# Performance work log

Measured on AMD Instinct MI355X. Metric: run time of the kernel, lower is better.

Reference implementation:

```python
import jax, jax.numpy as jnp
import numpy as np
from jax import lax

B = 64          # batch
IMG = 384       # image H=W
PATCH = 16      # stem patch size -> 24x24 grid
C = 192         # hidden_channels
K = 5           # knn_graph k (hard-coded in extract_graph)
HG = IMG // PATCH
N = HG * HG     # total_num_nodes = 576
HID = 4 * C     # FFN expansion
PRED_HID = 1024
NUM_CLASSES = 1


def setup_inputs() -> dict:
    key = jax.random.key(0)
    ks = jax.random.split(key, 16)
    def w(k, shape, s=0.02):
        return jax.random.normal(k, shape, jnp.float32) * s
    f32 = jnp.float32
    return {
        "x": jax.random.normal(ks[0], (B, 3, IMG, IMG), f32),
        # stem: 16x16 patch-embed conv
        "stem_w": w(ks[1], (C, 3, PATCH, PATCH)),
        "stem_b": jnp.zeros((C,), f32),
        "pos_embed": w(ks[2], (1, C, HG, HG)),
        # GSAT edge-attention MLP: concat(src,dst) -> C -> 1 -> sigmoid
        "att_w1": w(ks[3], (2 * C, C)), "att_b1": jnp.zeros((C,), f32),
        "att_w2": w(ks[4], (C, 1)),     "att_b2": jnp.zeros((1,), f32),
        # two message-passing layers (GIN-style update)
        "gnn_w1": w(ks[5], (C, C)), "gnn_b1": jnp.zeros((C,), f32),
        "gnn_w2": w(ks[6], (C, C)), "gnn_b2": jnp.zeros((C,), f32),
        # FFN (1x1 convs == channel matmuls), BN in eval mode (mean0/var1)
        "ffn_w1": w(ks[7], (C, HID)), "ffn_b1": jnp.zeros((HID,), f32),
        "ffn_g1": jnp.ones((HID,), f32), "ffn_be1": jnp.zeros((HID,), f32),
        "ffn_w2": w(ks[8], (HID, C)), "ffn_b2": jnp.zeros((C,), f32),
        "ffn_g2": jnp.ones((C,), f32), "ffn_be2": jnp.zeros((C,), f32),
        # prediction head: 1x1 conv C->1024, BN(eval), gelu, 1x1 conv 1024->num_classes
        "pred_w1": w(ks[9], (C, PRED_HID)), "pred_b1": jnp.zeros((PRED_HID,), f32),
        "pred_g": jnp.ones((PRED_HID,), f32), "pred_be": jnp.zeros((PRED_HID,), f32),
        "pred_w2": w(ks[10], (PRED_HID, NUM_CLASSES)), "pred_b2": jnp.zeros((NUM_CLASSES,), f32),
    }


def reference(x, stem_w, stem_b, pos_embed,
              att_w1, att_b1, att_w2, att_b2,
              gnn_w1, gnn_b1, gnn_w2, gnn_b2,
              ffn_w1, ffn_b1, ffn_g1, ffn_be1,
              ffn_w2, ffn_b2, ffn_g2, ffn_be2,
              pred_w1, pred_b1, pred_g, pred_be, pred_w2, pred_b2):
    # ---- stem + pos_embed ----
    feat = lax.conv_general_dilated(x, stem_w, (PATCH, PATCH), 'VALID',
                                    dimension_numbers=('NCHW', 'OIHW', 'NCHW'))
    feat = feat + stem_b[None, :, None, None] + pos_embed        # [B,C,Hg,Wg]
    b, c, hg, wg = feat.shape
    n = hg * wg
    nf = feat.reshape(b, c, n).transpose(0, 2, 1)                # [B,N,C]
    nfd = lax.stop_gradient(nf)                                  # extract_graph under no_grad

    # ---- kNN graph build: per-image pairwise sq. distances + top-k ----
    sq = jnp.sum(nfd * nfd, axis=-1)                             # [B,N]
    d2 = sq[:, :, None] + sq[:, None, :] - 2.0 * jnp.einsum('bnc,bmc->bnm', nfd, nfd)
    d2 = d2 + jnp.eye(n, dtype=d2.dtype) * 1e9                   # exclude self-loops
    _, idx = lax.top_k(-d2, K)                                   # [B,N,K] nearest neighbors
    src = (idx + (jnp.arange(b) * n)[:, None, None]).reshape(-1)  # [E] global neighbor idx
    dst = jnp.repeat(jnp.arange(b * n), K)                        # [E] global center idx

    # ---- GSAT GNN: edge attention + attention-weighted message passing ----
    h = nfd.reshape(b * n, c)                                    # [BN,C] (detached)
    e = jax.nn.relu(jnp.concatenate([h[src], h[dst]], axis=-1) @ att_w1 + att_b1)
    edge_att = jax.nn.sigmoid(e @ att_w2 + att_b2)               # [E,1]
    for Wg, bg in ((gnn_w1, gnn_b1), (gnn_w2, gnn_b2)):
        m = jax.ops.segment_sum(edge_att * h[src], dst, num_segments=b * n)
        h = jax.nn.relu((h + m) @ Wg + bg)                       # GIN-style update

    # ---- FFN (1x1 convs) with residual, BN eval-mode affine ----
    t = h.reshape(b, n, c)                                       # [B,N,C]
    u = jax.nn.gelu((t @ ffn_w1 + ffn_b1) * ffn_g1 + ffn_be1, approximate=False)
    t = t + ((u @ ffn_w2 + ffn_b2) * ffn_g2 + ffn_be2)

    # ---- global average pool + prediction head ----
    g = jnp.mean(t, axis=1)                                      # [B,C]
    p = jax.nn.gelu((g @ pred_w1 + pred_b1) * pred_g + pred_be, approximate=False)
    prediction = p @ pred_w2 + pred_b2                           # [B,num_classes]
    return edge_att, prediction
```

## Files before the change

kernel.cpp:

```cpp
#include <hip/hip_runtime.h>
#include <hip/hip_bf16.h>
#include <math.h>

constexpr int B_    = 64;
constexpr int C_    = 192;
constexpr int N_    = 576;
constexpr int BN_   = B_ * N_;
constexpr int K_    = 5;
constexpr int E_    = BN_ * K_;

__device__ __forceinline__ float gelu_exact(float x) {
    return 0.5f * x * (1.0f + erff(x * 0.70710678118654752440f));
}

__device__ __forceinline__ float bf2f(unsigned short v) {
    return __uint_as_float(((unsigned)v) << 16);
}
__device__ __forceinline__ unsigned short f2bf(float x) {
    __hip_bfloat16 h = __float2bfloat16(x);
    return *(unsigned short*)&h;
}

__global__ __launch_bounds__(256) void transpose_w_k(const float* __restrict__ w,
                                                     float* __restrict__ wt) {
    int gid = blockIdx.x * 256 + threadIdx.x;
    int k = gid / 192, oc = gid % 192;
    wt[gid] = w[oc * 768 + k];
}

__global__ __launch_bounds__(256) void stem_gemm96_k(
    const float* __restrict__ x, const float* __restrict__ Wt,
    const float* __restrict__ sb, const float* __restrict__ pos,
    float* __restrict__ nf)
{
    __shared__ float As[96][68];
    __shared__ float Ws[64][68];
    const int tid = threadIdx.x;
    const int tr = tid >> 4, tc = tid & 15;
    const int mb = blockIdx.x;
    const int nb = blockIdx.y;
    const int b  = mb / 6;
    const int n0 = (mb % 6) * 96;

    float4 acc[6];
    #pragma unroll
    for (int i = 0; i < 6; ++i) acc[i] = float4{0.f, 0.f, 0.f, 0.f};

    for (int kc = 0; kc < 768; kc += 64) {
        #pragma unroll
        for (int i = 0; i < 6; ++i) {
            int q = i * 256 + tid;
            int m = q >> 4, kq = q & 15;
            int k = kc + kq * 4;
            int ci = k >> 8, rem = k & 255, dy = rem >> 4, dx = rem & 15;
            int n = n0 + m, py = n / 24, px = n % 24;
            const float* src = &x[(((size_t)(b * 3 + ci) * 384) + py * 16 + dy) * 384
                                  + px * 16 + dx];
            *(float4*)&As[m][kq * 4] = *(const float4*)src;
        }
        #pragma unroll
        for (int i = 0; i < 4; ++i) {
            int q = i * 256 + tid;
            int m = q >> 4, kq = q & 15;
            *(float4*)&Ws[m][kq * 4] =
                *(const float4*)&Wt[(size_t)(kc + m) * 192 + nb * 64 + kq * 4];
        }
        __syncthreads();
        #pragma unroll
        for (int k4 = 0; k4 < 64; k4 += 4) {
            float4 a4[6], b4[4];
            #pragma unroll
            for (int i = 0; i < 6; ++i) a4[i] = *(const float4*)&As[tr * 6 + i][k4];
            #pragma unroll
            for (int kk = 0; kk < 4; ++kk) b4[kk] = *(const float4*)&Ws[k4 + kk][tc * 4];
            #pragma unroll
            for (int i = 0; i < 6; ++i) {
                const float av[4] = {a4[i].x, a4[i].y, a4[i].z, a4[i].w};
                #pragma unroll
                for (int kk = 0; kk < 4; ++kk) {
                    acc[i].x += av[kk] * b4[kk].x;
                    acc[i].y += av[kk] * b4[kk].y;
                    acc[i].z += av[kk] * b4[kk].z;
                    acc[i].w += av[kk] * b4[kk].w;
                }
            }
        }
        __syncthreads();
    }

    #pragma unroll
    for (int i = 0; i < 6; ++i) {
        int n = n0 + tr * 6 + i;
        int row = b * 576 + n;
        int oc0 = nb * 64 + tc * 4;
        float v[4] = {acc[i].x, acc[i].y, acc[i].z, acc[i].w};
        #pragma unroll
        for (int j = 0; j < 4; ++j) {
            int oc = oc0 + j;
            v[j] = v[j] + sb[oc] + pos[oc * 576 + n];
        }
        *(float4*)&nf[(size_t)row * 192 + oc0] = float4{v[0], v[1], v[2], v[3]};
    }
}

__global__ __launch_bounds__(256) void sq_k(const float* __restrict__ nf,
                                            float* __restrict__ sq) {
    int wid = threadIdx.x >> 6, lane = threadIdx.x & 63;
    int n = blockIdx.x * 4 + wid;
    const float* row = nf + (size_t)n * 192;
    float s = 0.f;
    #pragma unroll
    for (int c = 0; c < 3; ++c) { float v = row[lane + c * 64]; s += v * v; }
    #pragma unroll
    for (int off = 32; off; off >>= 1) s += __shfl_down(s, off);
    if (lane == 0) sq[n] = s;
}

__global__ void transpose_nf_k(const float* __restrict__ nf, float* __restrict__ nfT) {
    __shared__ float tile[32][33];
    int b = blockIdx.z;
    int n0 = blockIdx.x * 32, c0 = blockIdx.y * 32;
    int tx = threadIdx.x, ty = threadIdx.y;
    #pragma unroll
    for (int r = 0; r < 4; ++r) {
        int i = ty * 4 + r;
        tile[i][tx] = nf[((size_t)b * 576 + n0 + i) * 192 + c0 + tx];
    }
    __syncthreads();
    #pragma unroll
    for (int r = 0; r < 4; ++r) {
        int i = ty * 4 + r;
        nfT[((size_t)b * 192 + c0 + i) * 576 + n0 + tx] = tile[tx][i];
    }
}

__global__ __launch_bounds__(64) void knn_sym_k(
    const float* __restrict__ nfT, const float* __restrict__ sqn,
    float* __restrict__ candV, int* __restrict__ candI)
{
    __shared__ float smem[64 * 69];
    float* As  = smem;
    float* Bs  = smem + 2048;
    float* d2s = smem;

    const int tid = threadIdx.x;
    const int tr = tid >> 3, tc = tid & 7;
    const int b = blockIdx.y;
    int t = blockIdx.x;
    int bi = 0;
    while (t >= 9 - bi) { t -= 9 - bi; ++bi; }
    const int bj = bi + t;
    const int r0 = bi * 64, c0 = bj * 64;

    float acc[8][8];
    #pragma unroll
    for (int i = 0; i < 8; ++i)
        #pragma unroll
        for (int j = 0; j < 8; ++j) acc[i][j] = 0.f;

    for (int kc = 0; kc < 192; kc += 32) {
        #pragma unroll
        for (int i = 0; i < 8; ++i) {
            int q = i * 64 + tid;
            int k = q >> 4, c4 = (q & 15) * 4;
            const float* srow = &nfT[((size_t)(b * 192 + kc + k)) * 576];
            *(float4*)&As[k * 64 + c4] = *(const float4*)&srow[r0 + c4];
            *(float4*)&Bs[k * 64 + c4] = *(const float4*)&srow[c0 + c4];
        }
        __syncthreads();
        #pragma unroll 8
        for (int kk = 0; kk < 32; ++kk) {
            float4 a0 = *(const float4*)&As[kk * 64 + tr * 8];
            float4 a1 = *(const float4*)&As[kk * 64 + tr * 8 + 4];
            float4 b0 = *(const float4*)&Bs[kk * 64 + tc * 8];
            float4 b1 = *(const float4*)&Bs[kk * 64 + tc * 8 + 4];
            const float av[8] = {a0.x, a0.y, a0.z, a0.w, a1.x, a1.y, a1.z, a1.w};
            const float bv[8] = {b0.x, b0.y, b0.z, b0.w, b1.x, b1.y, b1.z, b1.w};
            #pragma unroll
            for (int i = 0; i < 8; ++i)
                #pragma unroll
                for (int j = 0; j < 8; ++j)
                    acc[i][j] += av[i] * bv[j];
        }
        __syncthreads();
    }

    #pragma unroll
    for (int i = 0; i < 8; ++i) {
        int rl = tr * 8 + i, rg = r0 + rl;
        float sr = sqn[b * 576 + rg];
        #pragma unroll
        for (int j = 0; j < 8; ++j) {
            int cl = tc * 8 + j, cg = c0 + cl;
            float d = sr + sqn[b * 576 + cg] - 2.f * acc[i][j];
            if (cg == rg) d += 1e9f;
            d2s[rl * 69 + cl] = d;
        }
    }
    __syncthreads();

    {
        const int r = tid;
        float tv[5]; int ti[5];
        #pragma unroll
        for (int p = 0; p < 5; ++p) { tv[p] = 3.4e38f; ti[p] = 0; }
        for (int c = 0; c < 64; ++c) {
            float cv = d2s[r * 69 + c];
            if (cv < tv[4]) {
                int ci = c0 + c;
                #pragma unroll
                for (int q = 0; q < 5; ++q) {
                    bool less = cv < tv[q];
                    float nv = less ? tv[q] : cv;
                    int ni   = less ? ti[q] : ci;
                    tv[q] = less ? cv : tv[q];
                    ti[q] = less ? ci : ti[q];
                    cv = nv; ci = ni;
                }
            }
        }
        int gr = b * 576 + r0 + r;
        #pragma unroll
        for (int p = 0; p < 5; ++p) {
            candV[(size_t)gr * 45 + bj * 5 + p] = tv[p];
            candI[(size_t)gr * 45 + bj * 5 + p] = ti[p];
        }
    }

    if (bi != bj) {
        const int c = tid;
        float tv[5]; int ti[5];
        #pragma unroll
        for (int p = 0; p < 5; ++p) { tv[p] = 3.4e38f; ti[p] = 0; }
        for (int r = 0; r < 64; ++r) {
            float cv = d2s[r * 69 + c];
            if (cv < tv[4]) {
                int ci = r0 + r;
                #pragma unroll
                for (int q = 0; q < 5; ++q) {
                    bool less = cv < tv[q];
                    float nv = less ? tv[q] : cv;
                    int ni   = less ? ti[q] : ci;
                    tv[q] = less ? cv : tv[q];
                    ti[q] = less ? ci : ti[q];
                    cv = nv; ci = ni;
                }
            }
        }
        int gr = b * 576 + c0 + c;
        #pragma unroll
        for (int p = 0; p < 5; ++p) {
            candV[(size_t)gr * 45 + bi * 5 + p] = tv[p];
            candI[(size_t)gr * 45 + bi * 5 + p] = ti[p];
        }
    }
}

__global__ __launch_bounds__(256) void knn_merge_k(
    const float* __restrict__ candV, const int* __restrict__ candI,
    int* __restrict__ idxOut)
{
    int r = blockIdx.x * 256 + threadIdx.x;
    float tv[5]; int ti[5];
    #pragma unroll
    for (int p = 0; p < 5; ++p) { tv[p] = 3.4e38f; ti[p] = 0; }
    #pragma unroll 5
    for (int s = 0; s < 45; ++s) {
        float cv = candV[(size_t)r * 45 + s];
        if (cv < tv[4]) {
            int cidx = candI[(size_t)r * 45 + s];
            #pragma unroll
            for (int q = 0; q < 5; ++q) {
                bool less = cv < tv[q];
                float nv = less ? tv[q] : cv;
                int ni   = less ? ti[q] : cidx;
                tv[q] = less ? cv : tv[q];
                ti[q] = less ? cidx : ti[q];
                cv = nv; cidx = ni;
            }
        }
    }
    int base = (r / 576) * 576;
    #pragma unroll
    for (int p = 0; p < 5; ++p) idxOut[r * 5 + p] = base + ti[p];
}

template <int EPI>
__global__ __launch_bounds__(256) void gemm_rm_k(
    const float* __restrict__ A, const float* __restrict__ W, float* __restrict__ out,
    int M, int N, int K,
    const float* __restrict__ bias, const float* __restrict__ gsc,
    const float* __restrict__ gsh, const float* __restrict__ res)
{
    __shared__ float As[64][68];
    __shared__ float Ws[64][68];
    const int tid = threadIdx.x;
    const int tr = tid >> 4, tc = tid & 15;
    const int mBase = blockIdx.x * 64, nBase = blockIdx.y * 64;

    float4 acc[4];
    acc[0] = acc[1] = acc[2] = acc[3] = float4{0.f, 0.f, 0.f, 0.f};

    for (int kc = 0; kc < K; kc += 64) {
        #pragma unroll
        for (int i = 0; i < 4; ++i) {
            int q = i * 256 + tid;
            int m = q >> 4, kq = q & 15;
            *(float4*)&As[m][kq * 4] =
                *(const float4*)&A[(size_t)(mBase + m) * K + kc + kq * 4];
            *(float4*)&Ws[m][kq * 4] =
                *(const float4*)&W[(size_t)(kc + m) * N + nBase + kq * 4];
        }
        __syncthreads();
        #pragma unroll
        for (int k4 = 0; k4 < 64; k4 += 4) {
            float4 a4[4], b4[4];
            #pragma unroll
            for (int i = 0; i < 4; ++i) a4[i] = *(const float4*)&As[tr * 4 + i][k4];
            #pragma unroll
            for (int kk = 0; kk < 4; ++kk) b4[kk] = *(const float4*)&Ws[k4 + kk][tc * 4];
            #pragma unroll
            for (int i = 0; i < 4; ++i) {
                const float av[4] = {a4[i].x, a4[i].y, a4[i].z, a4[i].w};
                #pragma unroll
                for (int kk = 0; kk < 4; ++kk) {
                    acc[i].x += av[kk] * b4[kk].x;
                    acc[i].y += av[kk] * b4[kk].y;
                    acc[i].z += av[kk] * b4[kk].z;
                    acc[i].w += av[kk] * b4[kk].w;
                }
            }
        }
        __syncthreads();
    }

    #pragma unroll
    for (int i = 0; i < 4; ++i) {
        int row = mBase + tr * 4 + i;
        int n0 = nBase + tc * 4;
        float v[4] = {acc[i].x, acc[i].y, acc[i].z, acc[i].w};
        #pragma unroll
        for (int j = 0; j < 4; ++j) {
            int n = n0 + j;
            float xv = v[j];
            if (EPI == 1) xv += bias[n];
            if (EPI == 2) { xv += bias[n]; xv = fmaxf(xv, 0.f); }
            if (EPI == 3) { xv = (xv + bias[n]) * gsc[n] + gsh[n]; xv = gelu_exact(xv); }
            if (EPI == 4) {
                xv = res[(size_t)row * N + n] + (xv + bias[n]) * gsc[n] + gsh[n];
            }
            v[j] = xv;
        }
        *(float4*)&out[(size_t)row * N + n0] = float4{v[0], v[1], v[2], v[3]};
    }
}

template <int EPI>
__global__ __launch_bounds__(256) void gemm_mfma_k(
    const unsigned short* __restrict__ A, const unsigned short* __restrict__ Bt,
    unsigned short* __restrict__ out, int M, int N, int K,
    const float* __restrict__ bias, const float* __restrict__ gsc,
    const float* __restrict__ gsh, const unsigned short* __restrict__ res)
{
    using frag = __attribute__((ext_vector_type(8))) short;
    using facc = __attribute__((ext_vector_type(4))) float;
    __shared__ unsigned short As[64][72];
    __shared__ unsigned short Bs[64][72];
    const int tid = threadIdx.x;
    const int wave = tid >> 6, lane = tid & 63;
    const int m16 = lane & 15, quad = lane >> 4;
    const int mBase = blockIdx.x * 64, nBase = blockIdx.y * 64;

    facc zero = {0.f, 0.f, 0.f, 0.f};
    facc acc[4];
    #pragma unroll
    for (int t = 0; t < 4; ++t) acc[t] = zero;

    for (int kc = 0; kc < K; kc += 64) {
        #pragma unroll
        for (int r = 0; r < 2; ++r) {
            int q = r * 256 + tid;
            int row = q >> 3, c8 = (q & 7) * 8;
            *(int4*)&As[row][c8] =
                *(const int4*)&A[(size_t)(mBase + row) * K + kc + c8];
            *(int4*)&Bs[row][c8] =
                *(const int4*)&Bt[(size_t)(nBase + row) * K + kc + c8];
        }
        __syncthreads();
        #pragma unroll
        for (int kk = 0; kk < 64; kk += 32) {
            frag a = *(const frag*)&As[16 * wave + m16][kk + quad * 8];
            #pragma unroll
            for (int t = 0; t < 4; ++t) {
                frag b = *(const frag*)&Bs[t * 16 + m16][kk + quad * 8];
                acc[t] = __builtin_amdgcn_mfma_f32_16x16x32_bf16(a, b, acc[t], 0, 0, 0);
            }
        }
        __syncthreads();
    }

    #pragma unroll
    for (int t = 0; t < 4; ++t) {
        #pragma unroll
        for (int r = 0; r < 4; ++r) {
            int row = mBase + 16 * wave + quad * 4 + r;
            int col = nBase + t * 16 + m16;
            float xv = acc[t][r];
            if (EPI == 2) { xv += bias[col]; xv = fmaxf(xv, 0.f); }
            if (EPI == 3) { xv = (xv + bias[col]) * gsc[col] + gsh[col]; xv = gelu_exact(xv); }
            if (EPI == 4) {
                xv = bf2f(res[(size_t)row * N + col]) + (xv + bias[col]) * gsc[col] + gsh[col];
            }
            out[(size_t)row * N + col] = f2bf(xv);
        }
    }
}

template <int EPI>
__global__ __launch_bounds__(256) void gemm_mfma_split_k(
    const unsigned short* __restrict__ Ah, const unsigned short* __restrict__ Al,
    const unsigned short* __restrict__ Bh, const unsigned short* __restrict__ Bl,
    float* __restrict__ out, int M, int N, int K, const float* __restrict__ bias)
{
    using frag = __attribute__((ext_vector_type(8))) short;
    using facc = __attribute__((ext_vector_type(4))) float;
    __shared__ unsigned short AsH[64][72], AsL[64][72];
    __shared__ unsigned short BsH[64][72], BsL[64][72];
    const int tid = threadIdx.x;
    const int wave = tid >> 6, lane = tid & 63;
    const int m16 = lane & 15, quad = lane >> 4;
    const int mBase = blockIdx.x * 64, nBase = blockIdx.y * 64;

    facc zero = {0.f, 0.f, 0.f, 0.f};
    facc acc[4];
    #pragma unroll
    for (int t = 0; t < 4; ++t) acc[t] = zero;

    for (int kc = 0; kc < K; kc += 64) {
        #pragma unroll
        for (int r = 0; r < 2; ++r) {
            int q = r * 256 + tid;
            int row = q >> 3, c8 = (q & 7) * 8;
            *(int4*)&AsH[row][c8] = *(const int4*)&Ah[(size_t)(mBase + row) * K + kc + c8];
            *(int4*)&AsL[row][c8] = *(const int4*)&Al[(size_t)(mBase + row) * K + kc + c8];
            *(int4*)&BsH[row][c8] = *(const int4*)&Bh[(size_t)(nBase + row) * K + kc + c8];
            *(int4*)&BsL[row][c8] = *(const int4*)&Bl[(size_t)(nBase + row) * K + kc + c8];
        }
        __syncthreads();
        #pragma unroll
        for (int kk = 0; kk < 64; kk += 32) {
            frag ah = *(const frag*)&AsH[16 * wave + m16][kk + quad * 8];
            frag al = *(const frag*)&AsL[16 * wave + m16][kk + quad * 8];
            #pragma unroll
            for (int t = 0; t < 4; ++t) {
                frag bh = *(const frag*)&BsH[t * 16 + m16][kk + quad * 8];
                frag bl = *(const frag*)&BsL[t * 16 + m16][kk + quad * 8];
                acc[t] = __builtin_amdgcn_mfma_f32_16x16x32_bf16(ah, bh, acc[t], 0, 0, 0);
                acc[t] = __builtin_amdgcn_mfma_f32_16x16x32_bf16(ah, bl, acc[t], 0, 0, 0);
                acc[t] = __builtin_amdgcn_mfma_f32_16x16x32_bf16(al, bh, acc[t], 0, 0, 0);
            }
        }
        __syncthreads();
    }

    #pragma unroll
    for (int t = 0; t < 4; ++t) {
        #pragma unroll
        for (int r = 0; r < 4; ++r) {
            int row = mBase + 16 * wave + quad * 4 + r;
            int col = nBase + t * 16 + m16;
            float xv = acc[t][r];
            if (EPI == 1) xv += bias[col];
            out[(size_t)row * N + col] = xv;
        }
    }
}

__global__ __launch_bounds__(256) void asplit_k(const float* __restrict__ a,
                                                unsigned short* __restrict__ hi,
                                                unsigned short* __restrict__ lo) {
    int g = blockIdx.x * 256 + threadIdx.x;
    float v = a[g];
    unsigned short h = f2bf(v);
    hi[g] = h;
    lo[g] = f2bf(v - bf2f(h));
}

__global__ __launch_bounds__(256) void wsplit_att_k(const float* __restrict__ w,
                                                    unsigned short* __restrict__ hi,
                                                    unsigned short* __restrict__ lo) {
    int gid = blockIdx.x * 256 + threadIdx.x;
    int half = gid / 36864, r = gid % 36864;
    int n = r / 192, k = r % 192;
    float v = w[(size_t)(half * 192 + k) * 192 + n];
    unsigned short h = f2bf(v);
    hi[gid] = h;
    lo[gid] = f2bf(v - bf2f(h));
}

__global__ __launch_bounds__(256) void wprep_k(const float* __restrict__ w,
                                               unsigned short* __restrict__ wt,
                                               int K, int N) {
    int gid = blockIdx.x * 256 + threadIdx.x;
    int n = gid / K, k = gid % K;
    wt[gid] = f2bf(w[(size_t)k * N + n]);
}

__global__ __launch_bounds__(256) void edge_att_k(
    const float* __restrict__ hA, const float* __restrict__ hB,
    const int* __restrict__ idx, const float* __restrict__ w2,
    const float* __restrict__ b2, float* __restrict__ att)
{
    int wid = threadIdx.x >> 6, lane = threadIdx.x & 63;
    int e = blockIdx.x * 4 + wid;
    int dst = e / K_;
    int src = idx[e];
    float s = 0.f;
    #pragma unroll
    for (int c0 = 0; c0 < 3; ++c0) {
        int c = lane + c0 * 64;
        float v = hA[(size_t)src * 192 + c] + hB[(size_t)dst * 192 + c];
        v = fmaxf(v, 0.f);
        s += v * w2[c];
    }
    #pragma unroll
    for (int off = 32; off; off >>= 1) s += __shfl_down(s, off);
    if (lane == 0) att[e] = 1.f / (1.f + expf(-(s + b2[0])));
}

__device__ __forceinline__ float ldv(const float* p, size_t i) { return p[i]; }
__device__ __forceinline__ float ldv(const unsigned short* p, size_t i) { return bf2f(p[i]); }

template <typename TI>
__global__ __launch_bounds__(256) void msg_bf_k(
    const TI* __restrict__ h, const float* __restrict__ att,
    const int* __restrict__ idx, unsigned short* __restrict__ s)
{
    int g = blockIdx.x * 256 + threadIdx.x;
    int n = g / 192, c = g % 192;
    float acc = ldv(h, (size_t)g);
    #pragma unroll
    for (int p = 0; p < K_; ++p) {
        int sp = idx[n * K_ + p];
        acc += att[n * K_ + p] * ldv(h, (size_t)sp * 192 + c);
    }
    s[g] = f2bf(acc);
}

__global__ void pool_bf16_k(const unsigned short* __restrict__ t, float* __restrict__ g) {
    int b = blockIdx.x, c = threadIdx.x;
    float s = 0.f;
    for (int n = 0; n < 576; ++n) s += bf2f(t[((size_t)b * 576 + n) * 192 + c]);
    g[b * 192 + c] = s * (1.f / 576.f);
}

__global__ __launch_bounds__(256) void head2_k(
    const float* __restrict__ p, const float* __restrict__ w2,
    const float* __restrict__ b2, float* __restrict__ out)
{
    int b = blockIdx.x;
    float s = 0.f;
    for (int j = threadIdx.x; j < 1024; j += 256) s += p[(size_t)b * 1024 + j] * w2[j];
    #pragma unroll
    for (int off = 32; off; off >>= 1) s += __shfl_down(s, off);
    __shared__ float ls[4];
    int wid = threadIdx.x >> 6, lane = threadIdx.x & 63;
    if (lane == 0) ls[wid] = s;
    __syncthreads();
    if (threadIdx.x == 0) out[b] = ls[0] + ls[1] + ls[2] + ls[3] + b2[0];
}

extern "C" void kernel_launch(void* const* d_in, const int* in_sizes, int n_in,
                              void* d_out, int out_size, void* d_ws, size_t ws_size,
                              hipStream_t stream) {
    const float* x        = (const float*)d_in[0];
    const float* stem_w   = (const float*)d_in[1];
    const float* stem_b   = (const float*)d_in[2];
    const float* pos      = (const float*)d_in[3];
    const float* att_w1   = (const float*)d_in[4];
    const float* att_b1   = (const float*)d_in[5];
    const float* att_w2   = (const float*)d_in[6];
    const float* att_b2   = (const float*)d_in[7];
    const float* gnn_w1   = (const float*)d_in[8];
    const float* gnn_b1   = (const float*)d_in[9];
    const float* gnn_w2   = (const float*)d_in[10];
    const float* gnn_b2   = (const float*)d_in[11];
    const float* ffn_w1   = (const float*)d_in[12];
    const float* ffn_b1   = (const float*)d_in[13];
    const float* ffn_g1   = (const float*)d_in[14];
    const float* ffn_be1  = (const float*)d_in[15];
    const float* ffn_w2   = (const float*)d_in[16];
    const float* ffn_b2   = (const float*)d_in[17];
    const float* ffn_g2   = (const float*)d_in[18];
    const float* ffn_be2  = (const float*)d_in[19];
    const float* pred_w1  = (const float*)d_in[20];
    const float* pred_b1  = (const float*)d_in[21];
    const float* pred_g   = (const float*)d_in[22];
    const float* pred_be  = (const float*)d_in[23];
    const float* pred_w2  = (const float*)d_in[24];
    const float* pred_b2  = (const float*)d_in[25];

    float* ws = (float*)d_ws;
    const size_t RSZ = (size_t)BN_ * C_;
    float* R0 = ws;
    float* R1 = R0 + RSZ;
    float* R2 = R1 + RSZ;
    float* R3 = R2 + RSZ;
    float* sqb = R3 + RSZ;
    int*   idxb = (int*)(sqb + BN_);
    float* gb = (float*)(idxb + E_);
    float* pb = gb + 64 * C_;
    unsigned short* wg1T = (unsigned short*)(pb + 64 * 1024);
    unsigned short* wg2T = wg1T + 192 * 192;
    unsigned short* wf1T = wg2T + 192 * 192;
    unsigned short* wf2T = wf1T + 768 * 192;
    unsigned short* waHi = wf2T + 192 * 768;
    unsigned short* waLo = waHi + 2 * 192 * 192;

    float* candV = R1;
    int*   candI = (int*)(R1 + (size_t)BN_ * 45);

    unsigned short* Sb    = (unsigned short*)R1;
    unsigned short* Hb    = (unsigned short*)(R1 + RSZ / 2);
    unsigned short* Tb    = (unsigned short*)R2;
    unsigned short* ToutB = (unsigned short*)(R2 + RSZ / 2);
    unsigned short* Ahi   = (unsigned short*)R3;
    unsigned short* Alo   = Ahi + RSZ;
    unsigned short* Ub    = (unsigned short*)R3;

    float* att  = (float*)d_out;
    float* pred = att + E_;

    float* Wt = R3;

    wprep_k<<<144, 256, 0, stream>>>(gnn_w1, wg1T, 192, 192);
    wprep_k<<<144, 256, 0, stream>>>(gnn_w2, wg2T, 192, 192);
    wprep_k<<<576, 256, 0, stream>>>(ffn_w1, wf1T, 192, 768);
    wprep_k<<<576, 256, 0, stream>>>(ffn_w2, wf2T, 768, 192);
    wsplit_att_k<<<288, 256, 0, stream>>>(att_w1, waHi, waLo);

    transpose_w_k<<<576, 256, 0, stream>>>(stem_w, Wt);
    stem_gemm96_k<<<dim3(384, 3), 256, 0, stream>>>(x, Wt, stem_b, pos, R0);

    sq_k<<<BN_ / 4, 256, 0, stream>>>(R0, sqb);
    transpose_nf_k<<<dim3(18, 6, 64), dim3(32, 8), 0, stream>>>(R0, R3);
    knn_sym_k<<<dim3(45, 64), 64, 0, stream>>>(R3, sqb, candV, candI);
    knn_merge_k<<<BN_ / 256, 256, 0, stream>>>(candV, candI, idxb);

    asplit_k<<<BN_ * C_ / 256, 256, 0, stream>>>(R0, Ahi, Alo);
    gemm_mfma_split_k<0><<<dim3(576, 3), 256, 0, stream>>>(Ahi, Alo,
        waHi, waLo, R1, BN_, 192, 192, nullptr);
    gemm_mfma_split_k<1><<<dim3(576, 3), 256, 0, stream>>>(Ahi, Alo,
        waHi + 36864, waLo + 36864, R2, BN_, 192, 192, att_b1);
    edge_att_k<<<E_ / 4, 256, 0, stream>>>(R1, R2, idxb, att_w2, att_b2, att);

    msg_bf_k<float><<<BN_ * C_ / 256, 256, 0, stream>>>(R0, att, idxb, Sb);
    gemm_mfma_k<2><<<dim3(576, 3), 256, 0, stream>>>(Sb, wg1T, Hb,
        BN_, 192, 192, gnn_b1, nullptr, nullptr, nullptr);
    msg_bf_k<unsigned short><<<BN_ * C_ / 256, 256, 0, stream>>>(Hb, att, idxb, Sb);
    gemm_mfma_k<2><<<dim3(576, 3), 256, 0, stream>>>(Sb, wg2T, Tb,
        BN_, 192, 192, gnn_b2, nullptr, nullptr, nullptr);

    for (int ch = 0; ch < 2; ++ch) {
        const unsigned short* Ain = Tb + (size_t)ch * 18432 * 192;
        unsigned short* Tout = ToutB + (size_t)ch * 18432 * 192;
        gemm_mfma_k<3><<<dim3(288, 12), 256, 0, stream>>>(Ain, wf1T, Ub,
            18432, 768, 192, ffn_b1, ffn_g1, ffn_be1, nullptr);
        gemm_mfma_k<4><<<dim3(288, 3), 256, 0, stream>>>(Ub, wf2T, Tout,
            18432, 192, 768, ffn_b2, ffn_g2, ffn_be2, Ain);
    }

    pool_bf16_k<<<64, 192, 0, stream>>>(ToutB, gb);
    gemm_rm_k<3><<<dim3(1, 16), 256, 0, stream>>>(gb, pred_w1, pb,
        64, 1024, 192, pred_b1, pred_g, pred_be, nullptr);
    head2_k<<<64, 256, 0, stream>>>(pb, pred_w2, pred_b2, pred);
}
```

Before: 780.7 us.

## Retile stem GEMM with register prefetch and shrink kNN shared memory

The stem GEMM moves to 128-thread blocks, each computing a 96x96 output tile (6x12 per thread) with a K-chunk of 32. The next A chunk is prefetched into registers while the current chunk is computed, aiming for more reuse per thread and overlap of global loads with FMAs. The kNN tile kernel uses a 16-deep K chunk and computes the distance tile in two 32-row phases in a smaller LDS buffer. Row top-5 selection is split across two half-waves and merged with xor shuffles, which cuts LDS use for occupancy (launch bounds 64,4) at the cost of extra syncs and shuffle work. The merge breaks ties by index, which may change how ties are ordered.

Measured after the change: 1.209 ms. 1.55x slower.

```diff
diff --git a/kernel.cpp b/kernel.cpp
--- a/kernel.cpp
+++ b/kernel.cpp
@@ -28,60 +28,79 @@
     wt[gid] = w[oc * 768 + k];
 }
 
-__global__ __launch_bounds__(256) void stem_gemm96_k(
+__global__ __launch_bounds__(128, 3) void stem_gemm96c_k(
     const float* __restrict__ x, const float* __restrict__ Wt,
     const float* __restrict__ sb, const float* __restrict__ pos,
     float* __restrict__ nf)
 {
-    __shared__ float As[96][68];
-    __shared__ float Ws[64][68];
+    __shared__ float As[96][36];
+    __shared__ float Ws[32][100];
     const int tid = threadIdx.x;
-    const int tr = tid >> 4, tc = tid & 15;
+    const int tr = tid >> 3, tc = tid & 7;
     const int mb = blockIdx.x;
     const int nb = blockIdx.y;
     const int b  = mb / 6;
     const int n0 = (mb % 6) * 96;
 
-    float4 acc[6];
-    #pragma unroll
-    for (int i = 0; i < 6; ++i) acc[i] = float4{0.f, 0.f, 0.f, 0.f};
-
-    for (int kc = 0; kc < 768; kc += 64) {
+    float4 acc[6][3];
+    #pragma unroll
+    for (int i = 0; i < 6; ++i)
+        #pragma unroll
+        for (int g = 0; g < 3; ++g) acc[i][g] = float4{0.f, 0.f, 0.f, 0.f};
+
+    float4 aP[6];
+    auto loadA = [&](int kc) {
         #pragma unroll
         for (int i = 0; i < 6; ++i) {
-            int q = i * 256 + tid;
-            int m = q >> 4, kq = q & 15;
+            int q = i * 128 + tid;
+            int m = q >> 3, kq = q & 7;
             int k = kc + kq * 4;
             int ci = k >> 8, rem = k & 255, dy = rem >> 4, dx = rem & 15;
             int n = n0 + m, py = n / 24, px = n % 24;
-            const float* src = &x[(((size_t)(b * 3 + ci) * 384) + py * 16 + dy) * 384
-                                  + px * 16 + dx];
-            *(float4*)&As[m][kq * 4] = *(const float4*)src;
-        }
-        #pragma unroll
-        for (int i = 0; i < 4; ++i) {
-            int q = i * 256 + tid;
-            int m = q >> 4, kq = q & 15;
-            *(float4*)&Ws[m][kq * 4] =
-                *(const float4*)&Wt[(size_t)(kc + m) * 192 + nb * 64 + kq * 4];
-        }
-        __syncthreads();
-        #pragma unroll
-        for (int k4 = 0; k4 < 64; k4 += 4) {
-            float4 a4[6], b4[4];
+            aP[i] = *(const float4*)&x[(((size_t)(b * 3 + ci) * 384) + py * 16 + dy) * 384
+                                       + px * 16 + dx];
+        }
+    };
+
+    loadA(0);
+    for (int kc = 0; kc < 768; kc += 32) {
+        #pragma unroll
+        for (int i = 0; i < 6; ++i) {
+            int q = i * 128 + tid;
+            int m = q >> 3, kq = q & 7;
+            *(float4*)&As[m][kq * 4] = aP[i];
+        }
+        #pragma unroll
+        for (int i = 0; i < 6; ++i) {
+            int q = i * 128 + tid;
+            int wr = q / 24, c4 = (q % 24) * 4;
+            *(float4*)&Ws[wr][c4] =
+                *(const float4*)&Wt[(size_t)(kc + wr) * 192 + nb * 96 + c4];
+        }
+        __syncthreads();
+        if (kc + 32 < 768) loadA(kc + 32);
+        #pragma unroll
+        for (int k4 = 0; k4 < 32; k4 += 4) {
+            float4 a4[6];
             #pragma unroll
             for (int i = 0; i < 6; ++i) a4[i] = *(const float4*)&As[tr * 6 + i][k4];
             #pragma unroll
-            for (int kk = 0; kk < 4; ++kk) b4[kk] = *(const float4*)&Ws[k4 + kk][tc * 4];
-            #pragma unroll
-            for (int i = 0; i < 6; ++i) {
-                const float av[4] = {a4[i].x, a4[i].y, a4[i].z, a4[i].w};
+            for (int kk = 0; kk < 4; ++kk) {
+                float4 b4[3];
                 #pragma unroll
-                for (int kk = 0; kk < 4; ++kk) {
-                    acc[i].x += av[kk] * b4[kk].x;
-                    acc[i].y += av[kk] * b4[kk].y;
-                    acc[i].z += av[kk] * b4[kk].z;
-                    acc[i].w += av[kk] * b4[kk].w;
+                for (int g = 0; g < 3; ++g)
+                    b4[g] = *(const float4*)&Ws[k4 + kk][tc * 12 + g * 4];
+                #pragma unroll
+                for (int i = 0; i < 6; ++i) {
+                    const float av = (kk == 0) ? a4[i].x : (kk == 1) ? a4[i].y
+                                   : (kk == 2) ? a4[i].z : a4[i].w;
+                    #pragma unroll
+                    for (int g = 0; g < 3; ++g) {
+                        acc[i][g].x += av * b4[g].x;
+                        acc[i][g].y += av * b4[g].y;
+                        acc[i][g].z += av * b4[g].z;
+                        acc[i][g].w += av * b4[g].w;
+                    }
                 }
             }
         }
@@ -92,14 +111,17 @@
     for (int i = 0; i < 6; ++i) {
         int n = n0 + tr * 6 + i;
         int row = b * 576 + n;
-        int oc0 = nb * 64 + tc * 4;
-        float v[4] = {acc[i].x, acc[i].y, acc[i].z, acc[i].w};
-        #pragma unroll
-        for (int j = 0; j < 4; ++j) {
-            int oc = oc0 + j;
-            v[j] = v[j] + sb[oc] + pos[oc * 576 + n];
-        }
-        *(float4*)&nf[(size_t)row * 192 + oc0] = float4{v[0], v[1], v[2], v[3]};
+        #pragma unroll
+        for (int g = 0; g < 3; ++g) {
+            int oc0 = nb * 96 + tc * 12 + g * 4;
+            float v[4] = {acc[i][g].x, acc[i][g].y, acc[i][g].z, acc[i][g].w};
+            #pragma unroll
+            for (int j = 0; j < 4; ++j) {
+                int oc = oc0 + j;
+                v[j] = v[j] + sb[oc] + pos[oc * 576 + n];
+            }
+            *(float4*)&nf[(size_t)row * 192 + oc0] = float4{v[0], v[1], v[2], v[3]};
+        }
     }
 }
 
@@ -134,14 +156,49 @@
     }
 }
 
-__global__ __launch_bounds__(64) void knn_sym_k(
+__device__ __forceinline__ void ins5(float* tv, int* ti, float cv, int ci) {
+    #pragma unroll
+    for (int q = 0; q < 5; ++q) {
+        bool less = cv < tv[q];
+        float nv = less ? tv[q] : cv;
+        int ni   = less ? ti[q] : ci;
+        tv[q] = less ? cv : tv[q];
+        ti[q] = less ? ci : ti[q];
+        cv = nv; ci = ni;
+    }
+}
+__device__ __forceinline__ void merge5_xor(float* tv, int* ti, int mask) {
+    float ov[5]; int oi[5];
+    #pragma unroll
+    for (int p = 0; p < 5; ++p) {
+        ov[p] = __shfl_xor(tv[p], mask);
+        oi[p] = __shfl_xor(ti[p], mask);
+    }
+    #pragma unroll
+    for (int s = 0; s < 5; ++s) {
+        float cv = ov[s]; int ci = oi[s];
+        if (cv < tv[4] || (cv == tv[4] && ci < ti[4])) {
+            #pragma unroll
+            for (int q = 0; q < 5; ++q) {
+                bool less = (cv < tv[q]) || (cv == tv[q] && ci < ti[q]);
+                float nv = less ? tv[q] : cv;
+                int ni   = less ? ti[q] : ci;
+                tv[q] = less ? cv : tv[q];
+                ti[q] = less ? ci : ti[q];
+                cv = nv; ci = ni;
+            }
+        }
+    }
+}
+
+__global__ __launch_bounds__(64, 4) void knn_sym3_k(
     const float* __restrict__ nfT, const float* __restrict__ sqn,
     float* __restrict__ candV, int* __restrict__ candI)
 {
-    __shared__ float smem[64 * 69];
-    float* As  = smem;
-    float* Bs  = smem + 2048;
-    float* d2s = smem;
+    __shared__ float smem[2304];
+    float (*As)[64]  = (float(*)[64])smem;
+    float (*Bs)[64]  = (float(*)[64])(smem + 1024);
+    float (*d2s)[72] = (float(*)[72])smem;
 
     const int tid = threadIdx.x;
     const int tr = tid >> 3, tc = tid & 7;
@@ -150,7 +207,7 @@
     int bi = 0;
     while (t >= 9 - bi) { t -= 9 - bi; ++bi; }
     const int bj = bi + t;
-    const int r0 = bi * 64, c0 = bj * 64;
+    const int row0 = bi * 64, c0 = bj * 64;
 
     float acc[8][8];
     #pragma unroll
@@ -158,22 +215,22 @@
         #pragma unroll
         for (int j = 0; j < 8; ++j) acc[i][j] = 0.f;
 
-    for (int kc = 0; kc < 192; kc += 32) {
+    for (int kc = 0; kc < 192; kc += 16) {
         #pragma unroll
         for (int i = 0; i < 8; ++i) {
             int q = i * 64 + tid;
-            int k = q >> 4, c4 = (q & 15) * 4;
-            const float* srow = &nfT[((size_t)(b * 192 + kc + k)) * 576];
-            *(float4*)&As[k * 64 + c4] = *(const float4*)&srow[r0 + c4];
-            *(float4*)&Bs[k * 64 + c4] = *(const float4*)&srow[c0 + c4];
-        }
-        __syncthreads();
-        #pragma unroll 8
-        for (int kk = 0; kk < 32; ++kk) {
-            float4 a0 = *(const float4*)&As[kk * 64 + tr * 8];
-            float4 a1 = *(const float4*)&As[kk * 64 + tr * 8 + 4];
-            float4 b0 = *(const float4*)&Bs[kk * 64 + tc * 8];
-            float4 b1 = *(const float4*)&Bs[kk * 64 + tc * 8 + 4];
+            int rr = (q >> 4) & 15, c4 = (q & 15) * 4;
+            const float* srow = &nfT[((size_t)(b * 192 + kc + rr)) * 576];
+            if (i < 4) *(float4*)&As[rr][c4] = *(const float4*)&srow[row0 + c4];
+            else       *(float4*)&Bs[rr][c4] = *(const float4*)&srow[c0 + c4];
+        }
+        __syncthreads();
+        #pragma unroll
+        for (int kk = 0; kk < 16; ++kk) {
+            float4 a0 = *(const float4*)&As[kk][tr * 8];
+            float4 a1 = *(const float4*)&As[kk][tr * 8 + 4];
+            float4 b0 = *(const float4*)&Bs[kk][tc * 8];
+            float4 b1 = *(const float4*)&Bs[kk][tc * 8 + 4];
             const float av[8] = {a0.x, a0.y, a0.z, a0.w, a1.x, a1.y, a1.z, a1.w};
             const float bv[8] = {b0.x, b0.y, b0.z, b0.w, b1.x, b1.y, b1.z, b1.w};
             #pragma unroll
@@ -185,73 +242,67 @@
         __syncthreads();
     }
 
-    #pragma unroll
-    for (int i = 0; i < 8; ++i) {
-        int rl = tr * 8 + i, rg = r0 + rl;
-        float sr = sqn[b * 576 + rg];
-        #pragma unroll
-        for (int j = 0; j < 8; ++j) {
-            int cl = tc * 8 + j, cg = c0 + cl;
-            float d = sr + sqn[b * 576 + cg] - 2.f * acc[i][j];
-            if (cg == rg) d += 1e9f;
-            d2s[rl * 69 + cl] = d;
-        }
-    }
-    __syncthreads();
-
-    {
-        const int r = tid;
-        float tv[5]; int ti[5];
-        #pragma unroll
-        for (int p = 0; p < 5; ++p) { tv[p] = 3.4e38f; ti[p] = 0; }
-        for (int c = 0; c < 64; ++c) {
-            float cv = d2s[r * 69 + c];
-            if (cv < tv[4]) {
-                int ci = c0 + c;
+    float tvB[5]; int tiB[5];
+    #pragma unroll
+    for (int p = 0; p < 5; ++p) { tvB[p] = 3.4e38f; tiB[p] = 0x7fffffff; }
+
+    #pragma unroll
+    for (int ph = 0; ph < 2; ++ph) {
+        const int base = ph * 32;
+        if ((tr >> 2) == ph) {
+            const int trl = tr & 3;
+            #pragma unroll
+            for (int i = 0; i < 8; ++i) {
+                int rl = trl * 8 + i;
+                int rg = row0 + base + rl;
+                float sr = sqn[b * 576 + rg];
+                float dv[8];
                 #pragma unroll
-                for (int q = 0; q < 5; ++q) {
-                    bool less = cv < tv[q];
-                    float nv = less ? tv[q] : cv;
-                    int ni   = less ? ti[q] : ci;
-                    tv[q] = less ? cv : tv[q];
-                    ti[q] = less ? ci : ti[q];
-                    cv = nv; ci = ni;
+                for (int j = 0; j < 8; ++j) {
+                    int cg = c0 + tc * 8 + j;
+                    float d = sr + sqn[b * 576 + cg] - 2.f * acc[i][j];
+                    if (cg == rg) d += 1e9f;
+                    dv[j] = d;
                 }
-            }
-        }
-        int gr = b * 576 + r0 + r;
+                *(float4*)&d2s[rl][tc * 8]     = float4{dv[0], dv[1], dv[2], dv[3]};
+                *(float4*)&d2s[rl][tc * 8 + 4] = float4{dv[4], dv[5], dv[6], dv[7]};
+            }
+        }
+        __syncthreads();
+        {
+            const int arow = tid & 31, part = tid >> 5;
+            float pv[5]; int pi[5];
+            #pragma unroll
+            for (int q = 0; q < 5; ++q) { pv[q] = 3.4e38f; pi[q] = 0x7fffffff; }
+            for (int j = 0; j < 32; ++j) {
+                int cl = part * 32 + j;
+                float cv = d2s[arow][cl];
+                if (cv < pv[4]) ins5(pv, pi, cv, c0 + cl);
+            }
+            merge5_xor(pv, pi, 32);
+            if (part == 0) {
+                int gr = b * 576 + row0 + base + arow;
+                #pragma unroll
+                for (int p = 0; p < 5; ++p) {
+                    candV[(size_t)gr * 45 + bj * 5 + p] = pv[p];
+                    candI[(size_t)gr * 45 + bj * 5 + p] = pi[p];
+                }
+            }
+        }
+        if (bi != bj) {
+            for (int rr = 0; rr < 32; ++rr) {
+                float cv = d2s[rr][tid];
+                if (cv < tvB[4]) ins5(tvB, tiB, cv, row0 + base + rr);
+            }
+        }
+        __syncthreads();
+    }
+    if (bi != bj) {
+        int gr = b * 576 + c0 + tid;
         #pragma unroll
         for (int p = 0; p < 5; ++p) {
-            candV[(size_t)gr * 45 + bj * 5 + p] = tv[p];
-            candI[(size_t)gr * 45 + bj * 5 + p] = ti[p];
-        }
-    }
-
-    if (bi != bj) {
-        const int c = tid;
-        float tv[5]; int ti[5];
-        #pragma unroll
-        for (int p = 0; p < 5; ++p) { tv[p] = 3.4e38f; ti[p] = 0; }
-        for (int r = 0; r < 64; ++r) {
-            float cv = d2s[r * 69 + c];
-            if (cv < tv[4]) {
-                int ci = r0 + r;
-                #pragma unroll
-                for (int q = 0; q < 5; ++q) {
-                    bool less = cv < tv[q];
-                    float nv = less ? tv[q] : cv;
-                    int ni   = less ? ti[q] : ci;
-                    tv[q] = less ? cv : tv[q];
-                    ti[q] = less ? ci : ti[q];
-                    cv = nv; ci = ni;
-                }
-            }
-        }
-        int gr = b * 576 + c0 + c;
-        #pragma unroll
-        for (int p = 0; p < 5; ++p) {
-            candV[(size_t)gr * 45 + bi * 5 + p] = tv[p];
-            candI[(size_t)gr * 45 + bi * 5 + p] = ti[p];
+            candV[(size_t)gr * 45 + bi * 5 + p] = tvB[p];
+            candI[(size_t)gr * 45 + bi * 5 + p] = tiB[p];
         }
     }
 }
@@ -640,11 +691,11 @@
     wsplit_att_k<<<288, 256, 0, stream>>>(att_w1, waHi, waLo);
 
     transpose_w_k<<<576, 256, 0, stream>>>(stem_w, Wt);
-    stem_gemm96_k<<<dim3(384, 3), 256, 0, stream>>>(x, Wt, stem_b, pos, R0);
+    stem_gemm96c_k<<<dim3(384, 2), 128, 0, stream>>>(x, Wt, stem_b, pos, R0);
 
     sq_k<<<BN_ / 4, 256, 0, stream>>>(R0, sqb);
     transpose_nf_k<<<dim3(18, 6, 64), dim3(32, 8), 0, stream>>>(R0, R3);
-    knn_sym_k<<<dim3(45, 64), 64, 0, stream>>>(R3, sqb, candV, candI);
+    knn_sym3_k<<<dim3(45, 64), 64, 0, stream>>>(R3, sqb, candV, candI);
     knn_merge_k<<<BN_ / 256, 256, 0, stream>>>(candV, candI, idxb);
 
     asplit_k<<<BN_ * C_ / 256, 256, 0, stream>>>(R0, Ahi, Alo);
```

## Enlarge bf16 MFMA GEMM M-tile to 256 rows per block

Applied to the files above, without the earlier changes.

The bf16 MFMA GEMM now has each block cover 256 rows instead of 64. Each wave computes a 64x64 sub-tile with a 4x4 accumulator grid and reuses the B fragments across four A fragments. This cuts the number of times B tiles are reloaded, raises MFMA work per LDS load, and shrinks the grids by a factor of four. The cost is higher register and LDS use per block and fewer blocks, which may lower occupancy. The diff also adds a redundant duplicate store of candI in the knn kernel that has no speed purpose.

Result: no change. 773.6 us (-0.9%).

```diff
diff --git a/kernel.cpp b/kernel.cpp
--- a/kernel.cpp
+++ b/kernel.cpp
@@ -251,6 +251,10 @@
         #pragma unroll
         for (int p = 0; p < 5; ++p) {
             candV[(size_t)gr * 45 + bi * 5 + p] = tv[p];
+            candI[(size_t)gr * 45 + bi * 5 + p] = tv[p] == tv[p] ? ti[p] : ti[p];
+        }
+        #pragma unroll
+        for (int p = 0; p < 5; ++p) {
             candI[(size_t)gr * 45 + bi * 5 + p] = ti[p];
         }
     }
@@ -364,54 +368,69 @@
 {
     using frag = __attribute__((ext_vector_type(8))) short;
     using facc = __attribute__((ext_vector_type(4))) float;
-    __shared__ unsigned short As[64][72];
+    __shared__ unsigned short As[256][72];
     __shared__ unsigned short Bs[64][72];
     const int tid = threadIdx.x;
     const int wave = tid >> 6, lane = tid & 63;
     const int m16 = lane & 15, quad = lane >> 4;
-    const int mBase = blockIdx.x * 64, nBase = blockIdx.y * 64;
+    const int mBase = blockIdx.x * 256, nBase = blockIdx.y * 64;
 
     facc zero = {0.f, 0.f, 0.f, 0.f};
-    facc acc[4];
-    #pragma unroll
-    for (int t = 0; t < 4; ++t) acc[t] = zero;
+    facc acc[4][4];
+    #pragma unroll
+    for (int ms = 0; ms < 4; ++ms)
+        #pragma unroll
+        for (int t = 0; t < 4; ++t) acc[ms][t] = zero;
 
     for (int kc = 0; kc < K; kc += 64) {
         #pragma unroll
-        for (int r = 0; r < 2; ++r) {
+        for (int r = 0; r < 8; ++r) {
             int q = r * 256 + tid;
             int row = q >> 3, c8 = (q & 7) * 8;
             *(int4*)&As[row][c8] =
                 *(const int4*)&A[(size_t)(mBase + row) * K + kc + c8];
+        }
+        #pragma unroll
+        for (int r = 0; r < 2; ++r) {
+            int q = r * 256 + tid;
+            int row = q >> 3, c8 = (q & 7) * 8;
             *(int4*)&Bs[row][c8] =
                 *(const int4*)&Bt[(size_t)(nBase + row) * K + kc + c8];
         }
         __syncthreads();
         #pragma unroll
         for (int kk = 0; kk < 64; kk += 32) {
-            frag a = *(const frag*)&As[16 * wave + m16][kk + quad * 8];
-            #pragma unroll
-            for (int t = 0; t < 4; ++t) {
-                frag b = *(const frag*)&Bs[t * 16 + m16][kk + quad * 8];
-                acc[t] = __builtin_amdgcn_mfma_f32_16x16x32_bf16(a, b, acc[t], 0, 0, 0);
-            }
-        }
-        __syncthreads();
-    }
-
-    #pragma unroll
-    for (int t = 0; t < 4; ++t) {
-        #pragma unroll
-        for (int r = 0; r < 4; ++r) {
-            int row = mBase + 16 * wave + quad * 4 + r;
-            int col = nBase + t * 16 + m16;
-            float xv = acc[t][r];
-            if (EPI == 2) { xv += bias[col]; xv = fmaxf(xv, 0.f); }
-            if (EPI == 3) { xv = (xv + bias[col]) * gsc[col] + gsh[col]; xv = gelu_exact(xv); }
-            if (EPI == 4) {
-                xv = bf2f(res[(size_t)row * N + col]) + (xv + bias[col]) * gsc[col] + gsh[col];
-            }
-            out[(size_t)row * N + col] = f2bf(xv);
+            frag bfr[4];
+            #pragma unroll
+            for (int t = 0; t < 4; ++t)
+                bfr[t] = *(const frag*)&Bs[t * 16 + m16][kk + quad * 8];
+            #pragma unroll
+            for (int ms = 0; ms < 4; ++ms) {
+                frag a = *(const frag*)&As[64 * wave + ms * 16 + m16][kk + quad * 8];
+                #pragma unroll
+                for (int t = 0; t < 4; ++t)
+                    acc[ms][t] = __builtin_amdgcn_mfma_f32_16x16x32_bf16(a, bfr[t], acc[ms][t], 0, 0, 0);
+            }
+        }
+        __syncthreads();
+    }
+
+    #pragma unroll
+    for (int ms = 0; ms < 4; ++ms) {
+        #pragma unroll
+        for (int t = 0; t < 4; ++t) {
+            #pragma unroll
+            for (int r = 0; r < 4; ++r) {
+                int row = mBase + 64 * wave + ms * 16 + quad * 4 + r;
+                int col = nBase + t * 16 + m16;
+                float xv = acc[ms][t][r];
+                if (EPI == 2) { xv += bias[col]; xv = fmaxf(xv, 0.f); }
+                if (EPI == 3) { xv = (xv + bias[col]) * gsc[col] + gsh[col]; xv = gelu_exact(xv); }
+                if (EPI == 4) {
+                    xv = bf2f(res[(size_t)row * N + col]) + (xv + bias[col]) * gsc[col] + gsh[col];
+                }
+                out[(size_t)row * N + col] = f2bf(xv);
+            }
         }
     }
 }
@@ -655,18 +674,18 @@
     edge_att_k<<<E_ / 4, 256, 0, stream>>>(R1, R2, idxb, att_w2, att_b2, att);
 
     msg_bf_k<float><<<BN_ * C_ / 256, 256, 0, stream>>>(R0, att, idxb, Sb);
-    gemm_mfma_k<2><<<dim3(576, 3), 256, 0, stream>>>(Sb, wg1T, Hb,
+    gemm_mfma_k<2><<<dim3(144, 3), 256, 0, stream>>>(Sb, wg1T, Hb,
         BN_, 192, 192, gnn_b1, nullptr, nullptr, nullptr);
     msg_bf_k<unsigned short><<<BN_ * C_ / 256, 256, 0, stream>>>(Hb, att, idxb, Sb);
-    gemm_mfma_k<2><<<dim3(576, 3), 256, 0, stream>>>(Sb, wg2T, Tb,
+    gemm_mfma_k<2><<<dim3(144, 3), 256, 0, stream>>>(Sb, wg2T, Tb,
         BN_, 192, 192, gnn_b2, nullptr, nullptr, nullptr);
 
     for (int ch = 0; ch < 2; ++ch) {
         const unsigned short* Ain = Tb + (size_t)ch * 18432 * 192;
         unsigned short* Tout = ToutB + (size_t)ch * 18432 * 192;
-        gemm_mfma_k<3><<<dim3(288, 12), 256, 0, stream>>>(Ain, wf1T, Ub,
+        gemm_mfma_k<3><<<dim3(72, 12), 256, 0, stream>>>(Ain, wf1T, Ub,
             18432, 768, 192, ffn_b1, ffn_g1, ffn_be1, nullptr);
-        gemm_mfma_k<4><<<dim3(288, 3), 256, 0, stream>>>(Ub, wf2T, Tout,
+        gemm_mfma_k<4><<<dim3(72, 3), 256, 0, stream>>>(Ub, wf2T, Tout,
             18432, 192, 768, ffn_b2, ffn_g2, ffn_be2, Ain);
     }
 
```
